# Kernel tuning notes

Measured on AMD Instinct MI355X. Metric: run time of the kernel, lower is better.

## Reference

```python
import jax, jax.numpy as jnp
import numpy as np

NUM_ITERATIONS = 3


def squash(s, axis=-1):
    # s * sqrt(||s||^2) / (1 + ||s||^2), matching the torch source exactly
    sq = jnp.sum(s * s, axis=axis, keepdims=True)
    return s * jnp.sqrt(sq) / (1.0 + sq)


def setup_inputs() -> dict:
    key = jax.random.key(0)
    k_u, k_w = jax.random.split(key)
    B, J, R, O, I = 128, 166, 864, 8, 4
    u = jax.random.normal(k_u, (B, R, I), dtype=jnp.float32)
    W = jax.random.normal(k_w, (1, J, R, O, I), dtype=jnp.float32)
    return {"u": u, "W": W}


def reference(u, W):
    # u: [B, R, I]; W: [1, J, R, O, I]
    Wq = W[0]  # [J, R, O, I]
    # u_hat[b,j,r,o] = sum_i W[j,r,o,i] * u[b,r,i]
    u_hat = jnp.einsum('jroi,bri->bjro', Wq, u)  # [B, J, R, O]
    # routing logits start shared across batch (torch init: [1,J,R,1,1])
    b_ij = jnp.zeros((1, Wq.shape[0], Wq.shape[1]), dtype=u_hat.dtype)  # [1, J, R]
    v_j = None
    for it in range(NUM_ITERATIONS):
        c_ij = jax.nn.softmax(b_ij, axis=2)           # softmax over routes R
        s_j = jnp.einsum('bjr,bjro->bjo', jnp.broadcast_to(c_ij, u_hat.shape[:3]), u_hat)  # [B, J, O]
        v_j = squash(s_j, axis=-1)                    # [B, J, O]
        if it < NUM_ITERATIONS - 1:
            # agreement a[b,j,r] = <u_hat[b,j,r,:], v[b,j,:]>
            a_ij = jnp.einsum('bjro,bjo->bjr', u_hat, v_j)
            b_ij = b_ij + a_ij                        # broadcasts to [B, J, R]
    return v_j  # equivalent to torch v_j.squeeze() for B > 1
```

## Files before the change

### kernel.cpp

```cpp
#include <hip/hip_runtime.h>
#include <math.h>


#define BB 128
#define JJ 166
#define RR 864
#define OO 8
#define KMAX 14
#define CH_U2 2048

typedef __fp16 h2v __attribute__((ext_vector_type(2)));

__device__ __forceinline__ uint32_t pack2(float a, float b) {
    return __builtin_bit_cast(uint32_t, __builtin_amdgcn_cvt_pkrtz(a, b));
}
__device__ __forceinline__ h2v bc_h2(uint32_t u) {
    return __builtin_bit_cast(h2v, u);
}
__device__ __forceinline__ float lo_f(uint32_t u) {
    return (float)__builtin_bit_cast(h2v, u).x;
}
__device__ __forceinline__ float hi_f(uint32_t u) {
    return (float)__builtin_bit_cast(h2v, u).y;
}

__device__ __forceinline__ float wave_sum(float v) {
#pragma unroll
    for (int m = 32; m >= 1; m >>= 1) v += __shfl_xor(v, m, 64);
    return v;
}

#define WBLOCKS 4482
#define UBLOCKS 432
__global__ __launch_bounds__(256) void pack_kernel(
    const float4* __restrict__ W4, const float4* __restrict__ u4,
    uint2* __restrict__ Wp, uint2* __restrict__ up) {
    if (blockIdx.x < WBLOCKS) {
        const int t = blockIdx.x * 256 + threadIdx.x;
        const float4 w = W4[t];
        const int o = t & 7;
        const int jr = t >> 3;
        const int r = jr % RR;
        const int j = jr / RR;
        Wp[(j * OO + o) * RR + r] = make_uint2(pack2(w.x, w.y), pack2(w.z, w.w));
    } else {
        const int t = (blockIdx.x - WBLOCKS) * 256 + threadIdx.x;
        const float4 uu = u4[t];
        up[t] = make_uint2(pack2(uu.x, uu.y), pack2(uu.z, uu.w));
    }
}

__global__ __launch_bounds__(256) void digitcaps_kernel(
    const uint2* __restrict__ Wp, const uint2* __restrict__ up,
    float* __restrict__ out) {
    const int tid = threadIdx.x;
    const int lane = tid & 63;
    const int wave = tid >> 6;

    const int j = blockIdx.x >> 5;
    const int b = ((blockIdx.x & 31) << 2) + wave;

    __shared__ uint2 wlds[2][CH_U2];

    uint32_t uh[KMAX][4];

#define STAGE(CC, BUF, MASKED)                                                 \
    {                                                                          \
        const uint2* gch = Wp + j * (OO * RR) + (CC) * 256;                    \
        _Pragma("unroll")                                                      \
        for (int n = 0; n < 4; ++n) {                                          \
            const int lin2 = (n << 9) + (tid << 1);                            \
            const int o = lin2 >> 8;                                           \
            const int rl = lin2 & 255;                                         \
            if (!(MASKED) || rl < 96) {                                        \
                const uint2* gsrc = gch + o * RR + rl;                         \
                uint2* ldst = &wlds[BUF][(n << 9) + (wave << 7)];              \
                __builtin_amdgcn_global_load_lds(                              \
                    (const __attribute__((address_space(1))) uint32_t*)gsrc,   \
                    (__attribute__((address_space(3))) uint32_t*)ldst,         \
                    16, 0, 0);                                                 \
            }                                                                  \
        }                                                                      \
    }

#define COMPUTE(CC, BUF, KK)                                                   \
    {                                                                          \
        _Pragma("unroll")                                                      \
        for (int kl = 0; kl < (KK); ++kl) {                                    \
            const int rl = (kl << 6) + lane;                                   \
            const bool valid = ((CC) * 4 + kl < KMAX - 1) || (lane < 32);      \
            const int rloff = valid ? rl : 0;                                  \
            const uint2 uu = up[b * RR + (CC) * 256 + rloff];                  \
            float d[OO];                                                       \
            _Pragma("unroll")                                                  \
            for (int o = 0; o < OO; ++o) {                                     \
                const uint2 ww = wlds[BUF][(o << 8) + rl];                     \
                float t0 = __builtin_amdgcn_fdot2(bc_h2(ww.x), bc_h2(uu.x),    \
                                                  0.0f, false);                \
                d[o] = __builtin_amdgcn_fdot2(bc_h2(ww.y), bc_h2(uu.y), t0,    \
                                              false);                          \
            }                                                                  \
            _Pragma("unroll")                                                  \
            for (int o2 = 0; o2 < 4; ++o2)                                     \
                uh[(CC) * 4 + kl][o2] =                                        \
                    valid ? pack2(d[2 * o2], d[2 * o2 + 1]) : 0u;              \
        }                                                                      \
    }

    STAGE(0, 0, false)
    __syncthreads();
    STAGE(1, 1, false)
    COMPUTE(0, 0, 4)
    __syncthreads();
    STAGE(2, 0, false)
    COMPUTE(1, 1, 4)
    __syncthreads();
    STAGE(3, 1, true)
    COMPUTE(2, 0, 4)
    __syncthreads();
    COMPUTE(3, 1, 2)
#undef STAGE
#undef COMPUTE

    float V[OO];
    float v[OO];

    {
        h2v accp[4];
#pragma unroll
        for (int o2 = 0; o2 < 4; ++o2) accp[o2] = bc_h2(uh[0][o2]);
#pragma unroll
        for (int k = 1; k < KMAX; ++k)
#pragma unroll
            for (int o2 = 0; o2 < 4; ++o2) accp[o2] += bc_h2(uh[k][o2]);

        float s[OO];
#pragma unroll
        for (int o2 = 0; o2 < 4; ++o2) {
            s[2 * o2]     = wave_sum((float)accp[o2].x) * (1.0f / (float)RR);
            s[2 * o2 + 1] = wave_sum((float)accp[o2].y) * (1.0f / (float)RR);
        }
        float n2 = 0.0f;
#pragma unroll
        for (int o = 0; o < OO; ++o) n2 += s[o] * s[o];
        const float scale = sqrtf(n2) / (1.0f + n2);
#pragma unroll
        for (int o = 0; o < OO; ++o) { v[o] = s[o] * scale; V[o] = v[o]; }
    }

#pragma unroll
    for (int it = 1; it < 3; ++it) {
        uint32_t Vp[4];
#pragma unroll
        for (int o2 = 0; o2 < 4; ++o2)
            Vp[o2] = pack2(V[2 * o2], V[2 * o2 + 1]);

        float zp = 0.0f;
        float sp[OO];
#pragma unroll
        for (int o = 0; o < OO; ++o) sp[o] = 0.0f;

#pragma unroll
        for (int k = 0; k < KMAX; ++k) {
            float br = 0.0f;
#pragma unroll
            for (int o2 = 0; o2 < 4; ++o2)
                br = __builtin_amdgcn_fdot2(bc_h2(uh[k][o2]), bc_h2(Vp[o2]),
                                            br, false);
            const float e = (k < KMAX - 1 || lane < 32) ? __expf(br) : 0.0f;
            zp += e;
#pragma unroll
            for (int o2 = 0; o2 < 4; ++o2) {
                sp[2 * o2]     = fmaf(e, lo_f(uh[k][o2]), sp[2 * o2]);
                sp[2 * o2 + 1] = fmaf(e, hi_f(uh[k][o2]), sp[2 * o2 + 1]);
            }
        }
        const float invZ = 1.0f / wave_sum(zp);

        float s[OO];
#pragma unroll
        for (int o = 0; o < OO; ++o) s[o] = wave_sum(sp[o]) * invZ;

        float n2 = 0.0f;
#pragma unroll
        for (int o = 0; o < OO; ++o) n2 += s[o] * s[o];
        const float scale = sqrtf(n2) / (1.0f + n2);
#pragma unroll
        for (int o = 0; o < OO; ++o) v[o] = s[o] * scale;

        if (it < 2) {
#pragma unroll
            for (int o = 0; o < OO; ++o) V[o] += v[o];
        }
    }

    float outv = 0.0f;
#pragma unroll
    for (int o = 0; o < OO; ++o)
        if (lane == o) outv = v[o];
    if (lane < OO) out[(b * JJ + j) * OO + lane] = outv;
}

extern "C" void kernel_launch(void* const* d_in, const int* in_sizes, int n_in,
                              void* d_out, int out_size, void* d_ws, size_t ws_size,
                              hipStream_t stream) {
    const float* u = (const float*)d_in[0];
    const float* W = (const float*)d_in[1];
    float* out = (float*)d_out;

    uint2* Wp = (uint2*)d_ws;
    uint2* up = (uint2*)((char*)d_ws + 9179136);

    pack_kernel<<<WBLOCKS + UBLOCKS, 256, 0, stream>>>(
        (const float4*)W, (const float4*)u, Wp, up);

    const int grid = JJ * (BB / 4);
    digitcaps_kernel<<<grid, 256, 0, stream>>>(Wp, up, out);
}
```

Measured before the change: 149.9 us.

## Read fp32 u directly in main kernel and halve LDS chunk size

Drops the fp16 packing of u from the pack kernel and has the routing kernel load u as float4, converting to fp16 in registers. The W staging chunk is halved from 256 to 128 routes, so the double-buffered pipeline runs 7 stages instead of 4. This saves a pre-pass write and re-read of packed u and cuts LDS use, which may raise occupancy. In exchange each u load moves twice the bytes, there are extra conversion instructions, and more barriers.

```diff
diff --git a/kernel.cpp b/kernel.cpp
--- a/kernel.cpp
+++ b/kernel.cpp
@@ -7,7 +7,7 @@
 #define RR 864
 #define OO 8
 #define KMAX 14
-#define CH_U2 2048
+#define CH_U2 1024
 
 typedef __fp16 h2v __attribute__((ext_vector_type(2)));
 
@@ -31,27 +31,19 @@
 }
 
 #define WBLOCKS 4482
-#define UBLOCKS 432
 __global__ __launch_bounds__(256) void pack_kernel(
-    const float4* __restrict__ W4, const float4* __restrict__ u4,
-    uint2* __restrict__ Wp, uint2* __restrict__ up) {
-    if (blockIdx.x < WBLOCKS) {
-        const int t = blockIdx.x * 256 + threadIdx.x;
-        const float4 w = W4[t];
-        const int o = t & 7;
-        const int jr = t >> 3;
-        const int r = jr % RR;
-        const int j = jr / RR;
-        Wp[(j * OO + o) * RR + r] = make_uint2(pack2(w.x, w.y), pack2(w.z, w.w));
-    } else {
-        const int t = (blockIdx.x - WBLOCKS) * 256 + threadIdx.x;
-        const float4 uu = u4[t];
-        up[t] = make_uint2(pack2(uu.x, uu.y), pack2(uu.z, uu.w));
-    }
+    const float4* __restrict__ W4, uint2* __restrict__ Wp) {
+    const int t = blockIdx.x * 256 + threadIdx.x;
+    const float4 w = W4[t];
+    const int o = t & 7;
+    const int jr = t >> 3;
+    const int r = jr % RR;
+    const int j = jr / RR;
+    Wp[(j * OO + o) * RR + r] = make_uint2(pack2(w.x, w.y), pack2(w.z, w.w));
 }
 
 __global__ __launch_bounds__(256) void digitcaps_kernel(
-    const uint2* __restrict__ Wp, const uint2* __restrict__ up,
+    const uint2* __restrict__ Wp, const float* __restrict__ u,
     float* __restrict__ out) {
     const int tid = threadIdx.x;
     const int lane = tid & 63;
@@ -60,18 +52,20 @@
     const int j = blockIdx.x >> 5;
     const int b = ((blockIdx.x & 31) << 2) + wave;
 
+    const float4* __restrict__ u4 = (const float4*)u;
+
     __shared__ uint2 wlds[2][CH_U2];
 
     uint32_t uh[KMAX][4];
 
 #define STAGE(CC, BUF, MASKED)                                                 \
     {                                                                          \
-        const uint2* gch = Wp + j * (OO * RR) + (CC) * 256;                    \
+        const uint2* gch = Wp + j * (OO * RR) + (CC) * 128;                    \
         _Pragma("unroll")                                                      \
-        for (int n = 0; n < 4; ++n) {                                          \
+        for (int n = 0; n < 2; ++n) {                                          \
             const int lin2 = (n << 9) + (tid << 1);                            \
-            const int o = lin2 >> 8;                                           \
-            const int rl = lin2 & 255;                                         \
+            const int o = lin2 >> 7;                                           \
+            const int rl = lin2 & 127;                                         \
             if (!(MASKED) || rl < 96) {                                        \
                 const uint2* gsrc = gch + o * RR + rl;                         \
                 uint2* ldst = &wlds[BUF][(n << 9) + (wave << 7)];              \
@@ -88,21 +82,23 @@
         _Pragma("unroll")                                                      \
         for (int kl = 0; kl < (KK); ++kl) {                                    \
             const int rl = (kl << 6) + lane;                                   \
-            const bool valid = ((CC) * 4 + kl < KMAX - 1) || (lane < 32);      \
+            const bool valid = ((CC) * 2 + kl < KMAX - 1) || (lane < 32);      \
             const int rloff = valid ? rl : 0;                                  \
-            const uint2 uu = up[b * RR + (CC) * 256 + rloff];                  \
+            const float4 uu4 = u4[b * RR + (CC) * 128 + rloff];                \
+            const uint32_t up0 = pack2(uu4.x, uu4.y);                          \
+            const uint32_t up1 = pack2(uu4.z, uu4.w);                          \
             float d[OO];                                                       \
             _Pragma("unroll")                                                  \
             for (int o = 0; o < OO; ++o) {                                     \
-                const uint2 ww = wlds[BUF][(o << 8) + rl];                     \
-                float t0 = __builtin_amdgcn_fdot2(bc_h2(ww.x), bc_h2(uu.x),    \
+                const uint2 ww = wlds[BUF][(o << 7) + rl];                     \
+                float t0 = __builtin_amdgcn_fdot2(bc_h2(ww.x), bc_h2(up0),     \
                                                   0.0f, false);                \
-                d[o] = __builtin_amdgcn_fdot2(bc_h2(ww.y), bc_h2(uu.y), t0,    \
+                d[o] = __builtin_amdgcn_fdot2(bc_h2(ww.y), bc_h2(up1), t0,     \
                                               false);                          \
             }                                                                  \
             _Pragma("unroll")                                                  \
             for (int o2 = 0; o2 < 4; ++o2)                                     \
-                uh[(CC) * 4 + kl][o2] =                                        \
+                uh[(CC) * 2 + kl][o2] =                                        \
                     valid ? pack2(d[2 * o2], d[2 * o2 + 1]) : 0u;              \
         }                                                                      \
     }
@@ -110,15 +106,24 @@
     STAGE(0, 0, false)
     __syncthreads();
     STAGE(1, 1, false)
-    COMPUTE(0, 0, 4)
+    COMPUTE(0, 0, 2)
     __syncthreads();
     STAGE(2, 0, false)
-    COMPUTE(1, 1, 4)
-    __syncthreads();
-    STAGE(3, 1, true)
-    COMPUTE(2, 0, 4)
-    __syncthreads();
+    COMPUTE(1, 1, 2)
+    __syncthreads();
+    STAGE(3, 1, false)
+    COMPUTE(2, 0, 2)
+    __syncthreads();
+    STAGE(4, 0, false)
     COMPUTE(3, 1, 2)
+    __syncthreads();
+    STAGE(5, 1, false)
+    COMPUTE(4, 0, 2)
+    __syncthreads();
+    STAGE(6, 0, true)
+    COMPUTE(5, 1, 2)
+    __syncthreads();
+    COMPUTE(6, 0, 2)
 #undef STAGE
 #undef COMPUTE
 
@@ -209,11 +214,9 @@
     float* out = (float*)d_out;
 
     uint2* Wp = (uint2*)d_ws;
-    uint2* up = (uint2*)((char*)d_ws + 9179136);
-
-    pack_kernel<<<WBLOCKS + UBLOCKS, 256, 0, stream>>>(
-        (const float4*)W, (const float4*)u, Wp, up);
+
+    pack_kernel<<<WBLOCKS, 256, 0, stream>>>((const float4*)W, Wp);
 
     const int grid = JJ * (BB / 4);
-    digitcaps_kernel<<<grid, 256, 0, stream>>>(Wp, up, out);
-}
+    digitcaps_kernel<<<grid, 256, 0, stream>>>(Wp, u, out);
+}
```

New measurement: 149.9 us. Within noise of the previous version (+0.0%).
